# Performance work log

Hardware: AMD Instinct MI355X
Metric: run time of the kernel (lower is better)

The kernel has to match this reference:

```python
import jax, jax.numpy as jnp
import numpy as np

B, C4, N, L4 = 8, 64, 512, 12
CQ = C4 // 4  # conv output channels


def setup_inputs() -> dict:
    key = jax.random.key(0)
    k_x, k_wc, k_bc, k_wg, k_bg = jax.random.split(key, 5)
    x = jax.random.normal(k_x, (B, C4, N, L4), dtype=jnp.float32)
    # Conv2d(in_dim, in_dim//4, kernel_size=(1,1)) -> pointwise: weight (CQ, C4)
    W_conv = jax.random.normal(k_wc, (CQ, C4), dtype=jnp.float32) / np.sqrt(C4)
    b_conv = jax.random.normal(k_bc, (CQ,), dtype=jnp.float32) * 0.01
    # Linear(in_dim, in_dim)
    W_gcn = jax.random.normal(k_wg, (C4, C4), dtype=jnp.float32) / np.sqrt(C4)
    b_gcn = jax.random.normal(k_bg, (C4,), dtype=jnp.float32) * 0.01
    return {"x": x, "W_conv": W_conv, "b_conv": b_conv, "W_gcn": W_gcn, "b_gcn": b_gcn}


def reference(x, W_conv, b_conv, W_gcn, b_gcn):
    # --- SpatioTemporalCorrelationComputation ---
    # 1x1 conv over channels: (b,c4,n,l) -> (b,cq,n,l)
    Fc = jnp.einsum('oc,bcnl->bonl', W_conv, x) + b_conv[None, :, None, None]
    Fl = Fc[:, :, :, -1]                                   # b,cq,n (last time step)
    xy = jnp.einsum('bcn,bcmt->bnmt', Fl, Fc)              # b,n,n,l4
    xx = jnp.sqrt(jnp.einsum('bcn,bcn->bc', Fl, Fl))       # b,cq
    yy = jnp.sqrt(jnp.einsum('bcnt,bcnt->bc', Fc, Fc))     # b,cq
    l2 = jnp.einsum('bc,bc->b', xx, yy)[:, None, None, None]
    S = xy / l2                                            # b,n,n,l4

    # --- RelationalFeatureExtraction ---
    # Loop-based R[:, :, :, k] = sum_j S[:,k,None,:,j] * F4[:,:,:,j]
    # is exactly this single contraction (Se expansion never materialized):
    R = jnp.einsum('bknj,bcnj->bcnk', S, x)                # b,c4,n,n

    # --- GraphOperation ---
    A = jax.nn.relu(jnp.tanh(jnp.max(R, axis=1)))          # b,n,n
    xg = jnp.einsum('bcnk,bkn->bck', R, A)                 # b,c4,n
    # Linear over channel dim: Fg[b,o,k] = sum_c xg[b,c,k] W[o,c] + bias[o]
    Fg = jnp.einsum('bck,oc->bok', xg, W_gcn) + b_gcn[None, :, None]
    return Fg[..., None]                                   # b,c4,n,1
```

## Files before the change

kernel.cpp:

```cpp
#include <hip/hip_runtime.h>
#include <hip/hip_bf16.h>
#include <math.h>

#define B    8
#define C4   64
#define CQ   16
#define NN   512
#define L4   12
#define NCH1 8
#define KT   128

#define O_TH   0
#define O_TL   (O_TH + (size_t)B*1024*NN/2)
#define O_T2H  (O_TL + (size_t)B*1024*NN/2)
#define O_T2L  (O_T2H + (size_t)B*NN*1024/2)
#define O_FL   (O_T2L + (size_t)B*NN*1024/2)
#define O_FLTH (O_FL + (size_t)B*CQ*NN)
#define O_FLTL (O_FLTH + (size_t)B*NN*16/2)
#define O_XX   (O_FLTL + (size_t)B*NN*16/2)
#define O_YY   (O_XX + B*CQ)
#define O_L2   (O_YY + B*CQ)
#define O_AH   (O_L2 + 16)
#define O_AL   (O_AH + (size_t)B*NN*NN/2)
#define O_XG   (O_AL + (size_t)B*NN*NN/2)

typedef __attribute__((ext_vector_type(8))) short short8;
typedef __attribute__((ext_vector_type(4))) float floatx4;
typedef __attribute__((ext_vector_type(16))) float floatx16;

__device__ inline void split2(float x0, float x1, uint& hw, uint& lw) {
  uint u0 = __float_as_uint(x0), u1 = __float_as_uint(x1);
  uint h0 = u0 >> 16, h1 = u1 >> 16;
  float r0 = x0 - __uint_as_float(h0 << 16);
  float r1 = x1 - __uint_as_float(h1 << 16);
  hw = h0 | (h1 << 16);
  lw = (__float_as_uint(r0) >> 16) | ((__float_as_uint(r1) >> 16) << 16);
}

__global__ __launch_bounds__(256) void k1_fc(const float* __restrict__ x,
                                             const float* __restrict__ Wc,
                                             const float* __restrict__ bc,
                                             float* __restrict__ ws) {
  int blk = blockIdx.x;
  int b = blk >> 6;
  int n0 = (blk & 63) * NCH1;
  int t = threadIdx.x;
  __shared__ __align__(16) float xs[C4*NCH1*L4];
  __shared__ float wcs[CQ*65];
  __shared__ float bcs[CQ];
  __shared__ __align__(16) float fcs[NCH1*CQ*L4];

  for (int e = t; e < CQ*C4; e += 256) {
    int q = e >> 6, c = e & 63;
    wcs[q*65 + c] = Wc[e];
  }
  if (t < CQ) bcs[t] = bc[t];
  const float* xb = x + (size_t)b*C4*NN*L4 + (size_t)n0*L4;
  for (int f = t; f < (C4*NCH1*L4)/4; f += 256) {
    int c = f / (NCH1*L4/4);
    int r = f - c*(NCH1*L4/4);
    float4 v = *(const float4*)(xb + (size_t)c*NN*L4 + r*4);
    *(float4*)(xs + c*(NCH1*L4) + r*4) = v;
  }
  __syncthreads();
  {
    int q = t & 15, slot = t >> 4;
    float accv[6];
    #pragma unroll
    for (int i = 0; i < 6; ++i) accv[i] = bcs[q];
    for (int c = 0; c < C4; ++c) {
      float wv = wcs[q*65 + c];
      const float* xc = xs + c*(NCH1*L4);
      #pragma unroll
      for (int i = 0; i < 6; ++i) accv[i] += wv * xc[slot + 16*i];
    }
    #pragma unroll
    for (int i = 0; i < 6; ++i) {
      int nj = slot + 16*i;
      int nl = nj / L4, j = nj - nl*L4;
      fcs[nl*(CQ*L4) + q*L4 + j] = accv[i];
      if (j == L4-1) ws[O_FL + ((size_t)b*CQ + q)*NN + n0 + nl] = accv[i];
    }
  }
  __syncthreads();
  if (t < CQ) {
    float yy = 0.f, xx = 0.f;
    for (int nl = 0; nl < NCH1; ++nl) {
      #pragma unroll
      for (int j = 0; j < L4; ++j) { float v = fcs[nl*(CQ*L4) + t*L4 + j]; yy += v*v; }
      float w = fcs[nl*(CQ*L4) + t*L4 + (L4-1)];
      xx += w*w;
    }
    atomicAdd(ws + O_YY + b*CQ + t, yy);
    atomicAdd(ws + O_XX + b*CQ + t, xx);
  }
  {
    int c = t >> 2, q0 = (t & 3) * 4;
    float vals[4][NCH1];
    ushort* T2H = (ushort*)(ws + O_T2H);
    ushort* T2L = (ushort*)(ws + O_T2L);
    for (int nl = 0; nl < NCH1; ++nl) {
      float xr[L4];
      *(float4*)&xr[0] = *(const float4*)(xs + c*(NCH1*L4) + nl*L4);
      *(float4*)&xr[4] = *(const float4*)(xs + c*(NCH1*L4) + nl*L4 + 4);
      *(float4*)&xr[8] = *(const float4*)(xs + c*(NCH1*L4) + nl*L4 + 8);
      float tvp[4];
      #pragma unroll
      for (int i = 0; i < 4; ++i) {
        float a = 0.f;
        #pragma unroll
        for (int j = 0; j < L4; ++j) a += fcs[nl*(CQ*L4) + (q0+i)*L4 + j] * xr[j];
        tvp[i] = a;
        vals[i][nl] = a;
      }
      uint hw0, lw0, hw1, lw1;
      split2(tvp[0], tvp[1], hw0, lw0);
      split2(tvp[2], tvp[3], hw1, lw1);
      size_t off2 = ((size_t)b*NN + n0 + nl)*1024 + t*4;
      *(uint2*)(T2H + off2) = make_uint2(hw0, hw1);
      *(uint2*)(T2L + off2) = make_uint2(lw0, lw1);
    }
    ushort* TH = (ushort*)(ws + O_TH);
    ushort* TL = (ushort*)(ws + O_TL);
    #pragma unroll
    for (int i = 0; i < 4; ++i) {
      int m = c*16 + q0 + i;
      uint hw[4], lw[4];
      #pragma unroll
      for (int jj = 0; jj < 4; ++jj)
        split2(vals[i][2*jj], vals[i][2*jj+1], hw[jj], lw[jj]);
      size_t off = ((size_t)b*1024 + m)*NN + n0;
      *(uint4*)(TH + off) = make_uint4(hw[0], hw[1], hw[2], hw[3]);
      *(uint4*)(TL + off) = make_uint4(lw[0], lw[1], lw[2], lw[3]);
    }
  }
}

__global__ __launch_bounds__(256) void k1b_l2flt(float* __restrict__ ws) {
  int t = threadIdx.x;
  if (blockIdx.x == 0) {
    __shared__ float s[B*CQ];
    if (t < B*CQ) s[t] = sqrtf(ws[O_XX + t]) * sqrtf(ws[O_YY + t]);
    __syncthreads();
    if (t < B) {
      float sum = 0.f;
      #pragma unroll
      for (int q = 0; q < CQ; ++q) sum += s[t*CQ + q];
      ws[O_L2 + t] = 1.0f / sum;
    }
  }
  int idx = blockIdx.x*256 + t;
  int b = idx >> 9, k = idx & 511;
  const float* fl = ws + O_FL + (size_t)b*CQ*NN + k;
  ushort h[16], l[16];
  #pragma unroll
  for (int q = 0; q < CQ; ++q) {
    float v = fl[(size_t)q*NN];
    uint u = __float_as_uint(v);
    uint hh = u >> 16;
    float r = v - __uint_as_float(hh << 16);
    h[q] = (ushort)hh;
    l[q] = (ushort)(__float_as_uint(r) >> 16);
  }
  ushort* FH  = (ushort*)(ws + O_FLTH) + (size_t)idx*16;
  ushort* FLo = (ushort*)(ws + O_FLTL) + (size_t)idx*16;
  *(uint4*)(FH)      = *(uint4*)&h[0];
  *(uint4*)(FH + 8)  = *(uint4*)&h[8];
  *(uint4*)(FLo)     = *(uint4*)&l[0];
  *(uint4*)(FLo + 8) = *(uint4*)&l[8];
}

__global__ __launch_bounds__(256, 4) void k2_mfma(float* __restrict__ ws) {
  int id = blockIdx.x;
  int b = id & 7;
  int rest = id >> 3;
  int kh = rest & 1;
  int nch = rest >> 1;
  int t = threadIdx.x;
  int w = t >> 6, lane = t & 63;
  int col = lane & 31, half = lane >> 5;
  float l2inv = ws[O_L2 + b];
  const ushort* FltH = (const ushort*)(ws + O_FLTH);
  const ushort* FltL = (const ushort*)(ws + O_FLTL);
  short8 bhf[2], blf[2];
  int kcol[2];
  #pragma unroll
  for (int kt = 0; kt < 2; ++kt) {
    kcol[kt] = kh*256 + w*64 + kt*32 + col;
    size_t off = ((size_t)(b*NN + kcol[kt]))*16 + half*8;
    bhf[kt] = *(const short8*)(FltH + off);
    blf[kt] = *(const short8*)(FltL + off);
  }
  const ushort* T2H = (const ushort*)(ws + O_T2H) + ((size_t)b*NN + nch*8)*1024;
  const ushort* T2L = (const ushort*)(ws + O_T2L) + ((size_t)b*NN + nch*8)*1024;
  ushort* AH = (ushort*)(ws + O_AH) + ((size_t)b*NN + nch*8)*NN;
  ushort* AL = (ushort*)(ws + O_AL) + ((size_t)b*NN + nch*8)*NN;

  for (int i = 0; i < 8; ++i) {
    short8 ah[2], al[2];
    #pragma unroll
    for (int ct = 0; ct < 2; ++ct) {
      size_t off = (size_t)i*1024 + (ct*32 + col)*16 + half*8;
      ah[ct] = *(const short8*)(T2H + off);
      al[ct] = *(const short8*)(T2L + off);
    }
    floatx16 acc[2][2];
    #pragma unroll
    for (int ct = 0; ct < 2; ++ct)
      #pragma unroll
      for (int kt = 0; kt < 2; ++kt) {
        floatx16 a = {0.f,0.f,0.f,0.f,0.f,0.f,0.f,0.f,
                      0.f,0.f,0.f,0.f,0.f,0.f,0.f,0.f};
        a = __builtin_amdgcn_mfma_f32_32x32x16_bf16(ah[ct], bhf[kt], a, 0, 0, 0);
        a = __builtin_amdgcn_mfma_f32_32x32x16_bf16(ah[ct], blf[kt], a, 0, 0, 0);
        a = __builtin_amdgcn_mfma_f32_32x32x16_bf16(al[ct], bhf[kt], a, 0, 0, 0);
        acc[ct][kt] = a;
      }
    #pragma unroll
    for (int kt = 0; kt < 2; ++kt) {
      float m = acc[0][kt][0];
      #pragma unroll
      for (int ct = 0; ct < 2; ++ct)
        #pragma unroll
        for (int rg = 0; rg < 16; ++rg)
          if (ct + rg) m = fmaxf(m, acc[ct][kt][rg]);
      m = fmaxf(m, __shfl_xor(m, 32));
      float av = fmaxf(tanhf(m*l2inv), 0.f);
      uint u = __float_as_uint(av);
      uint hh = u >> 16;
      float r = av - __uint_as_float(hh << 16);
      ushort lv = (ushort)(__float_as_uint(r) >> 16);
      if (half == 0) {
        AH[(size_t)i*NN + kcol[kt]] = (ushort)hh;
        AL[(size_t)i*NN + kcol[kt]] = lv;
      }
    }
  }
}

__global__ __launch_bounds__(256, 2) void k3_mfma(float* __restrict__ ws) {
  int id = blockIdx.x;
  int b = id & 7;
  int rest = id >> 3;
  int kb = rest & 7;
  int mbb = rest >> 3;
  int t = threadIdx.x;
  int lane = t & 63;
  int w = t >> 6;
  int mw = w >> 1, kw = w & 1;
  int row = lane & 15, quad = lane >> 4;

  __shared__ __align__(16) ushort Ah[128*32];
  __shared__ __align__(16) ushort Al[128*32];
  __shared__ __align__(16) ushort Bh[64*32];
  __shared__ __align__(16) ushort Bl[64*32];

  const ushort* TH = (const ushort*)(ws + O_TH) + ((size_t)b*1024 + mbb*128)*NN;
  const ushort* TL = (const ushort*)(ws + O_TL) + ((size_t)b*1024 + mbb*128)*NN;
  const ushort* AHp = (const ushort*)(ws + O_AH) + ((size_t)b*NN + kb*64)*NN;
  const ushort* ALp = (const ushort*)(ws + O_AL) + ((size_t)b*NN + kb*64)*NN;

  floatx4 acc[4][2];
  #pragma unroll
  for (int i = 0; i < 4; ++i)
    #pragma unroll
    for (int j = 0; j < 2; ++j) acc[i][j] = (floatx4){0.f, 0.f, 0.f, 0.f};

  for (int ksx = 0; ksx < 16; ++ksx) {
    int p0 = ksx*32;
    __syncthreads();
    #pragma unroll
    for (int i = 0; i < 2; ++i) {
      int f = t + 256*i;
      int m = f >> 2, seg = (f & 3) * 8;
      *(uint4*)(Ah + m*32 + seg) = *(const uint4*)(TH + (size_t)m*NN + p0 + seg);
      *(uint4*)(Al + m*32 + seg) = *(const uint4*)(TL + (size_t)m*NN + p0 + seg);
    }
    {
      int j = t >> 2, seg = (t & 3) * 8;
      *(uint4*)(Bh + j*32 + seg) = *(const uint4*)(AHp + (size_t)j*NN + p0 + seg);
      *(uint4*)(Bl + j*32 + seg) = *(const uint4*)(ALp + (size_t)j*NN + p0 + seg);
    }
    __syncthreads();
    short8 bh[2], bl[2];
    #pragma unroll
    for (int kt = 0; kt < 2; ++kt) {
      int jrow = kw*32 + kt*16 + row;
      bh[kt] = *(const short8*)(Bh + jrow*32 + quad*8);
      bl[kt] = *(const short8*)(Bl + jrow*32 + quad*8);
    }
    #pragma unroll
    for (int mt = 0; mt < 4; ++mt) {
      int mrow = mw*64 + mt*16 + row;
      short8 ah = *(const short8*)(Ah + mrow*32 + quad*8);
      short8 al = *(const short8*)(Al + mrow*32 + quad*8);
      #pragma unroll
      for (int kt = 0; kt < 2; ++kt) {
        acc[mt][kt] = __builtin_amdgcn_mfma_f32_16x16x32_bf16(ah, bh[kt], acc[mt][kt], 0, 0, 0);
        acc[mt][kt] = __builtin_amdgcn_mfma_f32_16x16x32_bf16(ah, bl[kt], acc[mt][kt], 0, 0, 0);
        acc[mt][kt] = __builtin_amdgcn_mfma_f32_16x16x32_bf16(al, bh[kt], acc[mt][kt], 0, 0, 0);
      }
    }
  }
  float l2inv = ws[O_L2 + b];
  const float* flb = ws + O_FL + (size_t)b*CQ*NN;
  float fl[2][4];
  #pragma unroll
  for (int kt = 0; kt < 2; ++kt) {
    int kcol = kb*64 + kw*32 + kt*16 + row;
    #pragma unroll
    for (int rg = 0; rg < 4; ++rg)
      fl[kt][rg] = flb[(size_t)(quad*4 + rg)*NN + kcol];
  }
  #pragma unroll
  for (int mt = 0; mt < 4; ++mt) {
    int c = mbb*8 + mw*4 + mt;
    #pragma unroll
    for (int kt = 0; kt < 2; ++kt) {
      float s = fl[kt][0]*acc[mt][kt][0] + fl[kt][1]*acc[mt][kt][1]
              + fl[kt][2]*acc[mt][kt][2] + fl[kt][3]*acc[mt][kt][3];
      s += __shfl_xor(s, 32);
      s += __shfl_xor(s, 16);
      if (quad == 0) {
        int kcol = kb*64 + kw*32 + kt*16 + row;
        ws[O_XG + ((size_t)b*C4 + c)*NN + kcol] = s * l2inv;
      }
    }
  }
}

__global__ __launch_bounds__(256) void k4_out(const float* __restrict__ Wg,
                                              const float* __restrict__ bg,
                                              const float* __restrict__ ws,
                                              float* __restrict__ out) {
  int blk = blockIdx.x;
  int b = blk >> 2, kc = blk & 3;
  int t = threadIdx.x;
  __shared__ float xg[C4][KT+1];
  __shared__ float wg[C4*C4];
  for (int e = t; e < C4*C4; e += 256) wg[e] = Wg[e];
  for (int e = t; e < C4*KT; e += 256) {
    int c = e >> 7, kk = e & (KT-1);
    xg[c][kk] = ws[O_XG + ((size_t)(b*C4 + c))*NN + kc*KT + kk];
  }
  __syncthreads();
  int kk = t & (KT-1);
  int ohalf = t >> 7;
  for (int oi = 0; oi < 32; ++oi) {
    int o = ohalf*32 + oi;
    float acc = bg[o];
    #pragma unroll
    for (int c = 0; c < C4; ++c) acc += wg[o*C4 + c] * xg[c][kk];
    out[((size_t)(b*C4 + o))*NN + kc*KT + kk] = acc;
  }
}

extern "C" void kernel_launch(void* const* d_in, const int* in_sizes, int n_in,
                              void* d_out, int out_size, void* d_ws, size_t ws_size,
                              hipStream_t stream) {
  const float* x  = (const float*)d_in[0];
  const float* Wc = (const float*)d_in[1];
  const float* bc = (const float*)d_in[2];
  const float* Wg = (const float*)d_in[3];
  const float* bg = (const float*)d_in[4];
  float* ws  = (float*)d_ws;
  float* out = (float*)d_out;

  hipMemsetAsync(ws + O_XX, 0, (2*B*CQ + 16)*sizeof(float), stream);

  k1_fc    <<<B*64,   256, 0, stream>>>(x, Wc, bc, ws);
  k1b_l2flt<<<16,     256, 0, stream>>>(ws);
  k2_mfma  <<<B*128,  256, 0, stream>>>(ws);
  k3_mfma  <<<B*64,   256, 0, stream>>>(ws);
  k4_out   <<<B*4,    256, 0, stream>>>(Wg, bg, ws, out);
}
```

Baseline: 153.7 us.

## Split Fc projection and T-tensor generation into separate kernels

Splits the first kernel into k1a_fc, which computes Fc and the norm partials and stores the Fc tile to global workspace, and k1t_T, which reloads x and that tile to build the split-bf16 T and T2 tensors. It also pads the shared-memory x rows to a stride of 100 to reduce LDS bank conflicts, and reorders block indexing so the batch index varies fastest. The aim is to cut register pressure and raise occupancy in the heavy T-generation phase (launch bounds 256,4). The cost is an extra kernel launch, a second read of x, and a round trip of Fc through global memory.

```diff
diff --git a/kernel.cpp b/kernel.cpp
--- a/kernel.cpp
+++ b/kernel.cpp
@@ -7,8 +7,8 @@
 #define CQ   16
 #define NN   512
 #define L4   12
-#define NCH1 8
 #define KT   128
+#define XSP  100
 
 #define O_TH   0
 #define O_TL   (O_TH + (size_t)B*1024*NN/2)
@@ -23,6 +23,7 @@
 #define O_AH   (O_L2 + 16)
 #define O_AL   (O_AH + (size_t)B*NN*NN/2)
 #define O_XG   (O_AL + (size_t)B*NN*NN/2)
+#define O_FCG  (O_XG + (size_t)B*C4*NN)
 
 typedef __attribute__((ext_vector_type(8))) short short8;
 typedef __attribute__((ext_vector_type(4))) float floatx4;
@@ -37,18 +38,19 @@
   lw = (__float_as_uint(r0) >> 16) | ((__float_as_uint(r1) >> 16) << 16);
 }
 
-__global__ __launch_bounds__(256) void k1_fc(const float* __restrict__ x,
-                                             const float* __restrict__ Wc,
-                                             const float* __restrict__ bc,
-                                             float* __restrict__ ws) {
-  int blk = blockIdx.x;
-  int b = blk >> 6;
-  int n0 = (blk & 63) * NCH1;
-  int t = threadIdx.x;
-  __shared__ __align__(16) float xs[C4*NCH1*L4];
+__global__ __launch_bounds__(256) void k1a_fc(const float* __restrict__ x,
+                                              const float* __restrict__ Wc,
+                                              const float* __restrict__ bc,
+                                              float* __restrict__ ws) {
+  int id = blockIdx.x;
+  int b = id & 7;
+  int nch = id >> 3;
+  int n0 = nch * 8;
+  int t = threadIdx.x;
+  __shared__ __align__(16) float xs[C4*XSP];
   __shared__ float wcs[CQ*65];
   __shared__ float bcs[CQ];
-  __shared__ __align__(16) float fcs[NCH1*CQ*L4];
+  __shared__ __align__(16) float fcs[8*CQ*L4];
 
   for (int e = t; e < CQ*C4; e += 256) {
     int q = e >> 6, c = e & 63;
@@ -56,11 +58,10 @@
   }
   if (t < CQ) bcs[t] = bc[t];
   const float* xb = x + (size_t)b*C4*NN*L4 + (size_t)n0*L4;
-  for (int f = t; f < (C4*NCH1*L4)/4; f += 256) {
-    int c = f / (NCH1*L4/4);
-    int r = f - c*(NCH1*L4/4);
+  for (int f = t; f < C4*24; f += 256) {
+    int c = f / 24, r = f - c*24;
     float4 v = *(const float4*)(xb + (size_t)c*NN*L4 + r*4);
-    *(float4*)(xs + c*(NCH1*L4) + r*4) = v;
+    *(float4*)(xs + c*XSP + r*4) = v;
   }
   __syncthreads();
   {
@@ -70,7 +71,7 @@
     for (int i = 0; i < 6; ++i) accv[i] = bcs[q];
     for (int c = 0; c < C4; ++c) {
       float wv = wcs[q*65 + c];
-      const float* xc = xs + c*(NCH1*L4);
+      const float* xc = xs + c*XSP;
       #pragma unroll
       for (int i = 0; i < 6; ++i) accv[i] += wv * xc[slot + 16*i];
     }
@@ -85,7 +86,7 @@
   __syncthreads();
   if (t < CQ) {
     float yy = 0.f, xx = 0.f;
-    for (int nl = 0; nl < NCH1; ++nl) {
+    for (int nl = 0; nl < 8; ++nl) {
       #pragma unroll
       for (int j = 0; j < L4; ++j) { float v = fcs[nl*(CQ*L4) + t*L4 + j]; yy += v*v; }
       float w = fcs[nl*(CQ*L4) + t*L4 + (L4-1)];
@@ -94,45 +95,70 @@
     atomicAdd(ws + O_YY + b*CQ + t, yy);
     atomicAdd(ws + O_XX + b*CQ + t, xx);
   }
+  float* fcg = ws + O_FCG + (size_t)(b*64 + nch)*1536;
+  for (int f = t; f < 384; f += 256)
+    *(float4*)(fcg + f*4) = *(const float4*)(fcs + f*4);
+}
+
+__global__ __launch_bounds__(256, 4) void k1t_T(const float* __restrict__ x,
+                                                float* __restrict__ ws) {
+  int id = blockIdx.x;
+  int b = id & 7;
+  int nch = id >> 3;
+  int n0 = nch * 8;
+  int t = threadIdx.x;
+  __shared__ __align__(16) float xs[C4*XSP];
+  __shared__ __align__(16) float fcs[8*CQ*L4];
+  const float* xb = x + (size_t)b*C4*NN*L4 + (size_t)n0*L4;
+  for (int f = t; f < C4*24; f += 256) {
+    int c = f / 24, r = f - c*24;
+    float4 v = *(const float4*)(xb + (size_t)c*NN*L4 + r*4);
+    *(float4*)(xs + c*XSP + r*4) = v;
+  }
   {
-    int c = t >> 2, q0 = (t & 3) * 4;
-    float vals[4][NCH1];
-    ushort* T2H = (ushort*)(ws + O_T2H);
-    ushort* T2L = (ushort*)(ws + O_T2L);
-    for (int nl = 0; nl < NCH1; ++nl) {
-      float xr[L4];
-      *(float4*)&xr[0] = *(const float4*)(xs + c*(NCH1*L4) + nl*L4);
-      *(float4*)&xr[4] = *(const float4*)(xs + c*(NCH1*L4) + nl*L4 + 4);
-      *(float4*)&xr[8] = *(const float4*)(xs + c*(NCH1*L4) + nl*L4 + 8);
-      float tvp[4];
-      #pragma unroll
-      for (int i = 0; i < 4; ++i) {
-        float a = 0.f;
-        #pragma unroll
-        for (int j = 0; j < L4; ++j) a += fcs[nl*(CQ*L4) + (q0+i)*L4 + j] * xr[j];
-        tvp[i] = a;
-        vals[i][nl] = a;
-      }
-      uint hw0, lw0, hw1, lw1;
-      split2(tvp[0], tvp[1], hw0, lw0);
-      split2(tvp[2], tvp[3], hw1, lw1);
-      size_t off2 = ((size_t)b*NN + n0 + nl)*1024 + t*4;
-      *(uint2*)(T2H + off2) = make_uint2(hw0, hw1);
-      *(uint2*)(T2L + off2) = make_uint2(lw0, lw1);
-    }
-    ushort* TH = (ushort*)(ws + O_TH);
-    ushort* TL = (ushort*)(ws + O_TL);
+    const float* fcg = ws + O_FCG + (size_t)(b*64 + nch)*1536;
+    for (int f = t; f < 384; f += 256)
+      *(float4*)(fcs + f*4) = *(const float4*)(fcg + f*4);
+  }
+  __syncthreads();
+  int c = t >> 2, q0 = (t & 3) * 4;
+  float vals[4][8];
+  ushort* T2H = (ushort*)(ws + O_T2H);
+  ushort* T2L = (ushort*)(ws + O_T2L);
+  for (int nl = 0; nl < 8; ++nl) {
+    float xr[L4];
+    *(float4*)&xr[0] = *(const float4*)(xs + c*XSP + nl*L4);
+    *(float4*)&xr[4] = *(const float4*)(xs + c*XSP + nl*L4 + 4);
+    *(float4*)&xr[8] = *(const float4*)(xs + c*XSP + nl*L4 + 8);
+    float tvp[4];
     #pragma unroll
     for (int i = 0; i < 4; ++i) {
-      int m = c*16 + q0 + i;
-      uint hw[4], lw[4];
-      #pragma unroll
-      for (int jj = 0; jj < 4; ++jj)
-        split2(vals[i][2*jj], vals[i][2*jj+1], hw[jj], lw[jj]);
-      size_t off = ((size_t)b*1024 + m)*NN + n0;
-      *(uint4*)(TH + off) = make_uint4(hw[0], hw[1], hw[2], hw[3]);
-      *(uint4*)(TL + off) = make_uint4(lw[0], lw[1], lw[2], lw[3]);
-    }
+      const float* fq = fcs + nl*(CQ*L4) + (q0+i)*L4;
+      float a = 0.f;
+      #pragma unroll
+      for (int j = 0; j < L4; ++j) a += fq[j] * xr[j];
+      tvp[i] = a;
+      vals[i][nl] = a;
+    }
+    uint hw0, lw0, hw1, lw1;
+    split2(tvp[0], tvp[1], hw0, lw0);
+    split2(tvp[2], tvp[3], hw1, lw1);
+    size_t off2 = ((size_t)b*NN + n0 + nl)*1024 + t*4;
+    *(uint2*)(T2H + off2) = make_uint2(hw0, hw1);
+    *(uint2*)(T2L + off2) = make_uint2(lw0, lw1);
+  }
+  ushort* TH = (ushort*)(ws + O_TH);
+  ushort* TL = (ushort*)(ws + O_TL);
+  #pragma unroll
+  for (int i = 0; i < 4; ++i) {
+    int m = c*16 + q0 + i;
+    uint hw[4], lw[4];
+    #pragma unroll
+    for (int jj = 0; jj < 4; ++jj)
+      split2(vals[i][2*jj], vals[i][2*jj+1], hw[jj], lw[jj]);
+    size_t off = ((size_t)b*1024 + m)*NN + n0;
+    *(uint4*)(TH + off) = make_uint4(hw[0], hw[1], hw[2], hw[3]);
+    *(uint4*)(TL + off) = make_uint4(lw[0], lw[1], lw[2], lw[3]);
   }
 }
 
@@ -368,8 +394,9 @@
 
   hipMemsetAsync(ws + O_XX, 0, (2*B*CQ + 16)*sizeof(float), stream);
 
-  k1_fc    <<<B*64,   256, 0, stream>>>(x, Wc, bc, ws);
+  k1a_fc   <<<B*64,   256, 0, stream>>>(x, Wc, bc, ws);
   k1b_l2flt<<<16,     256, 0, stream>>>(ws);
+  k1t_T    <<<B*64,   256, 0, stream>>>(x, ws);
   k2_mfma  <<<B*128,  256, 0, stream>>>(ws);
   k3_mfma  <<<B*64,   256, 0, stream>>>(ws);
   k4_out   <<<B*4,    256, 0, stream>>>(Wg, bg, ws, out);
```

After: 152.8 us. Within noise of the previous version (-0.6%).
